# Kernel tuning notes

Hardware: AMD Instinct MI355X
Metric: run time of the kernel (lower is better)

Reference implementation:

```python
import jax, jax.numpy as jnp
import numpy as np

D_MODEL = 512
D_VALUE = 512
N_HEADS = 8
NEG_INF = -1e30


def _layernorm(x, g, b, eps=1e-5):
    mu = jnp.mean(x, axis=-1, keepdims=True)
    var = jnp.var(x, axis=-1, keepdims=True)
    return (x - mu) * jax.lax.rsqrt(var + eps) * g + b


def setup_inputs() -> dict:
    key = jax.random.key(0)
    ks = jax.random.split(key, 16)
    B, L, dq = 4, 2048, 512
    d_model, d_value, H = D_MODEL, D_VALUE, N_HEADS
    d4 = 4 * d_model
    s = lambda d: 1.0 / np.sqrt(d)
    inp = {
        "q": jax.random.normal(ks[0], (B, L, dq), jnp.float32),
        "k": jax.random.normal(ks[1], (B, L, dq), jnp.float32),
        "v": jax.random.normal(ks[2], (B, L, d_value), jnp.float32),
        "Wq": jax.random.normal(ks[3], (d_model, dq), jnp.float32) * s(dq),
        "bq": jnp.zeros((d_model,), jnp.float32),
        "Wk": jax.random.normal(ks[4], (d_model, dq), jnp.float32) * s(dq),
        "bk": jnp.zeros((d_model,), jnp.float32),
        "Wv": jax.random.normal(ks[5], (d_model, d_value), jnp.float32) * s(d_value),
        "bv": jnp.zeros((d_model,), jnp.float32),
        "Wo": jax.random.normal(ks[6], (d_value, d_model), jnp.float32) * s(d_model),
        "bo": jnp.zeros((d_value,), jnp.float32),
        "Wc1": jax.random.normal(ks[7], (d4, d_value), jnp.float32) * s(d_value),
        "bc1": jnp.zeros((d4,), jnp.float32),
        "Wc2": jax.random.normal(ks[8], (d_value, d4), jnp.float32) * s(d4),
        "bc2": jnp.zeros((d_value,), jnp.float32),
        "g1": jnp.ones((d_value,), jnp.float32),
        "b1": jnp.zeros((d_value,), jnp.float32),
        "g2": jnp.ones((d_value,), jnp.float32),
        "b2": jnp.zeros((d_value,), jnp.float32),
        "Wl": jax.random.normal(ks[9], (d_model, d_value), jnp.float32) * s(d_value),
        "bl": jnp.zeros((d_model,), jnp.float32),
    }
    return inp


def reference(q, k, v, Wq, bq, Wk, bk, Wv, bv, Wo, bo, Wc1, bc1, Wc2, bc2,
              g1, b1, g2, b2, Wl, bl):
    B, L, _ = q.shape
    S = k.shape[1]
    H = N_HEADS
    E = D_MODEL // H
    # projections -> [B, L, H, E]
    queries = (q @ Wq.T + bq).reshape(B, L, H, E)
    keys = (k @ Wk.T + bk).reshape(B, S, H, E)
    values = (v @ Wv.T + bv).reshape(B, S, H, E)
    # naive causal attention, full [B,H,L,S] scores
    scale = 1.0 / np.sqrt(E)
    scores = jnp.einsum('blhe,bshe->bhls', queries, keys)
    causal = jnp.triu(jnp.ones((L, S), dtype=bool), k=1)  # True above diagonal
    scores = jnp.where(causal, NEG_INF, scores)
    A = jax.nn.softmax(scale * scores, axis=-1)
    att = jnp.einsum('bhls,bshd->blhd', A, values).reshape(B, L, H * E)
    att = att @ Wo.T + bo
    # residual + FFN (conv1d kernel_size=1 == pointwise linear)
    x = _layernorm(v + att, g1, b1)
    y = jax.nn.relu(x @ Wc1.T + bc1)
    y = y @ Wc2.T + bc2
    y = _layernorm(x + y, g2, b2)
    return y @ Wl.T + bl
```

## Files before the change

kernel.cpp:

```cpp
#include <hip/hip_runtime.h>
#include <hip/hip_bf16.h>


typedef __attribute__((ext_vector_type(8))) short sh8;
typedef __attribute__((ext_vector_type(4))) float f32x4;

#define QSCALE 0.18033688011110543f

__device__ __forceinline__ void storeOut(float* p, float v) { *p = v; }
__device__ __forceinline__ void storeOut(__hip_bfloat16* p, float v) { *p = __float2bfloat16(v); }

__device__ __forceinline__ void gl_lds16(const void* g, void* l) {
    __builtin_amdgcn_global_load_lds((const __attribute__((address_space(1))) void*)g,
                                     (__attribute__((address_space(3))) void*)l, 16, 0, 0);
}

__device__ __forceinline__ unsigned pk_bf16(float a, float b) {
    __hip_bfloat162 h = __float22bfloat162_rn(make_float2(a, b));
    return *(unsigned*)&h;
}
__device__ __forceinline__ sh8 pk8(float4 a, float4 b) {
    int4 iv = make_int4(pk_bf16(a.x, a.y), pk_bf16(a.z, a.w),
                        pk_bf16(b.x, b.y), pk_bf16(b.z, b.w));
    return *(sh8*)&iv;
}

struct WArg { const float* w[7]; unsigned short* wd; };
__global__ __launch_bounds__(256) void conv_w(WArg p)
{
    const int i = (blockIdx.x * 256 + threadIdx.x) * 4;
    if (i >= 3407872) return;
    const float* s; int off;
    if      (i < 262144)  { s = p.w[0]; off = i; }
    else if (i < 524288)  { s = p.w[1]; off = i - 262144; }
    else if (i < 786432)  { s = p.w[2]; off = i - 524288; }
    else if (i < 1048576) { s = p.w[3]; off = i - 786432; }
    else if (i < 1310720) { s = p.w[4]; off = i - 1048576; }
    else if (i < 2359296) { s = p.w[5]; off = i - 1310720; }
    else                  { s = p.w[6]; off = i - 2359296; }
    const float4 v = *(const float4*)(s + off);
    *(uint2*)(p.wd + i) = make_uint2(pk_bf16(v.x, v.y), pk_bf16(v.z, v.w));
}

struct QkvArg {
    const float *A0, *A1, *A2;
    const float *b0, *b1, *b2;
    unsigned short *C0, *C1;
    unsigned short *Vt;
};
__global__ __launch_bounds__(256) void gemm_qkv(QkvArg ar, const unsigned short* __restrict__ Wall,
                                                int M, int N, int K)
{
    const int z = blockIdx.z;
    const float* A = z == 0 ? ar.A0 : (z == 1 ? ar.A1 : ar.A2);
    const unsigned short* W = Wall + (size_t)z * 262144;
    const float* bias = z == 0 ? ar.b0 : (z == 1 ? ar.b1 : ar.b2);

    __shared__ float AsF[8192];
    __shared__ unsigned short BsL[8192];
    const int t    = threadIdx.x;
    const int wave = t >> 6, lane = t & 63;
    const int quad = lane >> 4, col = lane & 15;
    const int wm   = wave >> 1, wn = wave & 1;
    const int m0   = blockIdx.y * 128, n0 = blockIdx.x * 128;

    f32x4 acc[4][4];
    #pragma unroll
    for (int mt = 0; mt < 4; mt++)
        #pragma unroll
        for (int nt = 0; nt < 4; nt++)
            acc[mt][nt] = (f32x4){0.f, 0.f, 0.f, 0.f};

    for (int k0 = 0; k0 < K; k0 += 64) {
        #pragma unroll
        for (int seg = 0; seg < 8; seg++) {
            const int r0  = (seg * 4 + wave) * 4;
            const int row = r0 + (lane >> 4);
            const int ck  = (lane & 15) ^ (row & 15);
            gl_lds16(A + (size_t)(m0 + row) * K + k0 + ck * 4, &AsF[r0 * 64]);
        }
        #pragma unroll
        for (int seg = 0; seg < 4; seg++) {
            const int r0  = (seg * 4 + wave) * 8;
            const int row = r0 + (lane >> 3);
            const int ck  = (lane & 7) ^ (row & 7);
            gl_lds16(W + (size_t)(n0 + row) * K + k0 + ck * 8, &BsL[r0 * 64]);
        }
        __syncthreads();
        #pragma unroll
        for (int kc = 0; kc < 2; kc++) {
            sh8 af[4], bf[4];
            #pragma unroll
            for (int mt = 0; mt < 4; mt++) {
                const int mr  = wm * 64 + mt * 16 + col;
                const int q0  = kc * 8 + quad * 2;
                const int m16 = mr & 15;
                float4 f0 = *(const float4*)&AsF[mr * 64 + ((q0 ^ m16) << 2)];
                float4 f1 = *(const float4*)&AsF[mr * 64 + (((q0 + 1) ^ m16) << 2)];
                af[mt] = pk8(f0, f1);
            }
            #pragma unroll
            for (int nt = 0; nt < 4; nt++) {
                const int nr = wn * 64 + nt * 16 + col;
                bf[nt] = *(const sh8*)&BsL[nr * 64 + (((kc * 4 + quad) ^ (nr & 7)) << 3)];
            }
            #pragma unroll
            for (int mt = 0; mt < 4; mt++)
                #pragma unroll
                for (int nt = 0; nt < 4; nt++)
                    acc[mt][nt] = __builtin_amdgcn_mfma_f32_16x16x32_bf16(af[mt], bf[nt], acc[mt][nt], 0, 0, 0);
        }
        __syncthreads();
    }

    if (z < 2) {
        unsigned short* C = z == 0 ? ar.C0 : ar.C1;
        const float scale = z == 0 ? QSCALE : 1.0f;
        #pragma unroll
        for (int nt = 0; nt < 4; nt++) {
            const int cn = n0 + wn * 64 + nt * 16 + col;
            const float bj = bias[cn];
            #pragma unroll
            for (int mt = 0; mt < 4; mt++) {
                const int rm = m0 + wm * 64 + mt * 16 + quad * 4;
                #pragma unroll
                for (int reg = 0; reg < 4; reg++)
                    C[(size_t)(rm + reg) * N + cn] =
                        (unsigned short)__bfloat16_as_ushort(__float2bfloat16((acc[mt][nt][reg] + bj) * scale));
            }
        }
    } else {
        const int b = m0 >> 11;
        #pragma unroll
        for (int nt = 0; nt < 4; nt++) {
            const int cn = n0 + wn * 64 + nt * 16 + col;
            const int h = cn >> 6, e = cn & 63;
            const float bj = bias[cn];
            #pragma unroll
            for (int mt = 0; mt < 4; mt++) {
                const int s0r = (m0 + wm * 64 + mt * 16 + quad * 4) & 2047;
                float cv[4];
                #pragma unroll
                for (int reg = 0; reg < 4; reg++) cv[reg] = acc[mt][nt][reg] + bj;
                *(uint2*)(ar.Vt + ((size_t)(b * 8 + h) * 64 + e) * 2048 + s0r) =
                    make_uint2(pk_bf16(cv[0], cv[1]), pk_bf16(cv[2], cv[3]));
            }
        }
    }
}

template <typename TOUT, bool RELU>
__global__ __launch_bounds__(256) void gemm_mfma(const unsigned short* __restrict__ A,
                                                 const unsigned short* __restrict__ W,
                                                 const float* __restrict__ bias,
                                                 TOUT* __restrict__ C,
                                                 int M, int N, int K)
{
    __shared__ unsigned short AsL[8192];
    __shared__ unsigned short BsL[8192];
    const int t    = threadIdx.x;
    const int wave = t >> 6, lane = t & 63;
    const int quad = lane >> 4, col = lane & 15;
    const int wm   = wave >> 1, wn = wave & 1;
    const int m0   = blockIdx.y * 128, n0 = blockIdx.x * 128;

    f32x4 acc[4][4];
    #pragma unroll
    for (int mt = 0; mt < 4; mt++)
        #pragma unroll
        for (int nt = 0; nt < 4; nt++)
            acc[mt][nt] = (f32x4){0.f, 0.f, 0.f, 0.f};

    for (int k0 = 0; k0 < K; k0 += 64) {
        #pragma unroll
        for (int seg = 0; seg < 4; seg++) {
            const int r0  = (seg * 4 + wave) * 8;
            const int row = r0 + (lane >> 3);
            const int ck  = (lane & 7) ^ (row & 7);
            gl_lds16(A + (size_t)(m0 + row) * K + k0 + ck * 8, &AsL[r0 * 64]);
            gl_lds16(W + (size_t)(n0 + row) * K + k0 + ck * 8, &BsL[r0 * 64]);
        }
        __syncthreads();
        #pragma unroll
        for (int kc = 0; kc < 2; kc++) {
            sh8 af[4], bf[4];
            #pragma unroll
            for (int mt = 0; mt < 4; mt++) {
                const int ar = wm * 64 + mt * 16 + col;
                af[mt] = *(const sh8*)&AsL[ar * 64 + (((kc * 4 + quad) ^ (ar & 7)) << 3)];
            }
            #pragma unroll
            for (int nt = 0; nt < 4; nt++) {
                const int nr = wn * 64 + nt * 16 + col;
                bf[nt] = *(const sh8*)&BsL[nr * 64 + (((kc * 4 + quad) ^ (nr & 7)) << 3)];
            }
            #pragma unroll
            for (int mt = 0; mt < 4; mt++)
                #pragma unroll
                for (int nt = 0; nt < 4; nt++)
                    acc[mt][nt] = __builtin_amdgcn_mfma_f32_16x16x32_bf16(af[mt], bf[nt], acc[mt][nt], 0, 0, 0);
        }
        __syncthreads();
    }
    #pragma unroll
    for (int nt = 0; nt < 4; nt++) {
        const int cn = n0 + wn * 64 + nt * 16 + col;
        const float bj = bias[cn];
        #pragma unroll
        for (int mt = 0; mt < 4; mt++) {
            const int rm = m0 + wm * 64 + mt * 16 + quad * 4;
            #pragma unroll
            for (int reg = 0; reg < 4; reg++) {
                float cv = acc[mt][nt][reg] + bj;
                if (RELU) cv = fmaxf(cv, 0.f);
                storeOut(&C[(size_t)(rm + reg) * N + cn], cv);
            }
        }
    }
}

template <typename TOUT, bool RELU>
__global__ __launch_bounds__(256) void gemm_mfma64(const unsigned short* __restrict__ A,
                                                   const unsigned short* __restrict__ W,
                                                   const float* __restrict__ bias,
                                                   TOUT* __restrict__ C,
                                                   int M, int N, int K)
{
    __shared__ unsigned short AsL[4096];
    __shared__ unsigned short BsL[8192];
    const int t    = threadIdx.x;
    const int wave = t >> 6, lane = t & 63;
    const int quad = lane >> 4, col = lane & 15;
    const int wm   = wave >> 1, wn = wave & 1;
    const int m0   = blockIdx.y * 64, n0 = blockIdx.x * 128;

    f32x4 acc[2][4];
    #pragma unroll
    for (int mt = 0; mt < 2; mt++)
        #pragma unroll
        for (int nt = 0; nt < 4; nt++)
            acc[mt][nt] = (f32x4){0.f, 0.f, 0.f, 0.f};

    for (int k0 = 0; k0 < K; k0 += 64) {
        #pragma unroll
        for (int seg = 0; seg < 2; seg++) {
            const int r0  = (seg * 4 + wave) * 8;
            const int row = r0 + (lane >> 3);
            const int ck  = (lane & 7) ^ (row & 7);
            gl_lds16(A + (size_t)(m0 + row) * K + k0 + ck * 8, &AsL[r0 * 64]);
        }
        #pragma unroll
        for (int seg = 0; seg < 4; seg++) {
            const int r0  = (seg * 4 + wave) * 8;
            const int row = r0 + (lane >> 3);
            const int ck  = (lane & 7) ^ (row & 7);
            gl_lds16(W + (size_t)(n0 + row) * K + k0 + ck * 8, &BsL[r0 * 64]);
        }
        __syncthreads();
        #pragma unroll
        for (int kc = 0; kc < 2; kc++) {
            sh8 af[2], bf[4];
            #pragma unroll
            for (int mt = 0; mt < 2; mt++) {
                const int ar = wm * 32 + mt * 16 + col;
                af[mt] = *(const sh8*)&AsL[ar * 64 + (((kc * 4 + quad) ^ (ar & 7)) << 3)];
            }
            #pragma unroll
            for (int nt = 0; nt < 4; nt++) {
                const int nr = wn * 64 + nt * 16 + col;
                bf[nt] = *(const sh8*)&BsL[nr * 64 + (((kc * 4 + quad) ^ (nr & 7)) << 3)];
            }
            #pragma unroll
            for (int mt = 0; mt < 2; mt++)
                #pragma unroll
                for (int nt = 0; nt < 4; nt++)
                    acc[mt][nt] = __builtin_amdgcn_mfma_f32_16x16x32_bf16(af[mt], bf[nt], acc[mt][nt], 0, 0, 0);
        }
        __syncthreads();
    }
    #pragma unroll
    for (int nt = 0; nt < 4; nt++) {
        const int cn = n0 + wn * 64 + nt * 16 + col;
        const float bj = bias[cn];
        #pragma unroll
        for (int mt = 0; mt < 2; mt++) {
            const int rm = m0 + wm * 32 + mt * 16 + quad * 4;
            #pragma unroll
            for (int reg = 0; reg < 4; reg++) {
                float cv = acc[mt][nt][reg] + bj;
                if (RELU) cv = fmaxf(cv, 0.f);
                storeOut(&C[(size_t)(rm + reg) * N + cn], cv);
            }
        }
    }
}

__global__ __launch_bounds__(256, 2) void attn_mfma(const unsigned short* __restrict__ Qb,
                                                    const unsigned short* __restrict__ Kb,
                                                    const unsigned short* __restrict__ Vt,
                                                    float* __restrict__ Op,
                                                    float* __restrict__ Lp,
                                                    int L)
{
    __shared__ unsigned short Ks[4096];
    __shared__ unsigned short Vs[4096];
    __shared__ unsigned short Ps[4][16][72];

    const int x    = blockIdx.x;
    const int i    = x >> 1;
    const int sp   = x & 1;
    const int bh   = blockIdx.y;
    const int b    = bh >> 3, h = bh & 7;
    const int t    = threadIdx.x;
    const int w    = t >> 6, lane = t & 63;
    const int quad = lane >> 4, col = lane & 15;

    const int qtA = i, qtB = 31 - i;
    const int qrowA = qtA * 64 + w * 16 + col;
    const int qrowB = qtB * 64 + w * 16 + col;
    const int S  = 32 - i;
    const int h0 = (S + 1) >> 1;
    const int r0 = sp ? h0 : 0;
    const int r1 = sp ? S : h0;

    const int srow = lane >> 3;
    const int scp  = lane & 7;

    sh8 qfA[2], qfB[2];
    {
        const size_t qa = ((size_t)(b * L + qrowA) * 8 + h) * 64;
        qfA[0] = *(const sh8*)(Qb + qa + quad * 8);
        qfA[1] = *(const sh8*)(Qb + qa + 32 + quad * 8);
        const size_t qb2 = ((size_t)(b * L + qrowB) * 8 + h) * 64;
        qfB[0] = *(const sh8*)(Qb + qb2 + quad * 8);
        qfB[1] = *(const sh8*)(Qb + qb2 + 32 + quad * 8);
    }

    f32x4 OA[4], OB[4];
    #pragma unroll
    for (int nt = 0; nt < 4; nt++) { OA[nt] = (f32x4){0.f,0.f,0.f,0.f}; OB[nt] = (f32x4){0.f,0.f,0.f,0.f}; }
    float lA = 0.f, lB = 0.f;

    for (int r = r0; r < r1; r++) {
        const int k0 = r * 64;
        #pragma unroll
        for (int seg = 0; seg < 2; seg++) {
            const int rr  = (seg * 4 + w) * 8;
            const int row = rr + srow;
            const int ck  = scp ^ (row & 7);
            gl_lds16(Kb + ((size_t)(b * L + k0 + row) * 8 + h) * 64 + ck * 8, &Ks[rr * 64]);
            gl_lds16(Vt + (size_t)(bh * 64 + row) * L + k0 + ck * 8, &Vs[rr * 64]);
        }
        __syncthreads();

        const bool actA  = (r <= i);
        const bool maskA = (r == i);
        const bool maskB = (r == S - 1);

        f32x4 stA[4], stB[4];
        const f32x4 zz = {0.f, 0.f, 0.f, 0.f};
        #pragma unroll
        for (int ntk = 0; ntk < 4; ntk++) {
            const int key = ntk * 16 + col;
            const int sw  = key & 7;
            sh8 kf0 = *(const sh8*)&Ks[key * 64 + ((quad ^ sw) << 3)];
            sh8 kf1 = *(const sh8*)&Ks[key * 64 + (((quad + 4) ^ sw) << 3)];
            f32x4 aB = __builtin_amdgcn_mfma_f32_16x16x32_bf16(kf0, qfB[0], zz, 0, 0, 0);
            stB[ntk] = __builtin_amdgcn_mfma_f32_16x16x32_bf16(kf1, qfB[1], aB, 0, 0, 0);
            if (actA) {
                f32x4 aA = __builtin_amdgcn_mfma_f32_16x16x32_bf16(kf0, qfA[0], zz, 0, 0, 0);
                stA[ntk] = __builtin_amdgcn_mfma_f32_16x16x32_bf16(kf1, qfA[1], aA, 0, 0, 0);
            }
        }

        {
            if (maskB) {
                #pragma unroll
                for (int ntk = 0; ntk < 4; ntk++)
                    #pragma unroll
                    for (int reg = 0; reg < 4; reg++)
                        if (k0 + ntk * 16 + quad * 4 + reg > qrowB) stB[ntk][reg] = -1e30f;
            }
            #pragma unroll
            for (int ntk = 0; ntk < 4; ntk++) {
                #pragma unroll
                for (int reg = 0; reg < 4; reg++)
                    stB[ntk][reg] = exp2f(stB[ntk][reg]);
                lB += (stB[ntk][0] + stB[ntk][1]) + (stB[ntk][2] + stB[ntk][3]);
                *(uint2*)&Ps[w][col][ntk * 16 + quad * 4] =
                    make_uint2(pk_bf16(stB[ntk][0], stB[ntk][1]), pk_bf16(stB[ntk][2], stB[ntk][3]));
            }
            #pragma unroll
            for (int kchunk = 0; kchunk < 2; kchunk++) {
                sh8 pf = *(const sh8*)&Ps[w][col][kchunk * 32 + quad * 8];
                #pragma unroll
                for (int nt = 0; nt < 4; nt++) {
                    const int e = nt * 16 + col;
                    sh8 vf = *(const sh8*)&Vs[e * 64 + (((kchunk * 4 + quad) ^ (e & 7)) << 3)];
                    OB[nt] = __builtin_amdgcn_mfma_f32_16x16x32_bf16(pf, vf, OB[nt], 0, 0, 0);
                }
            }
        }

        if (actA) {
            if (maskA) {
                #pragma unroll
                for (int ntk = 0; ntk < 4; ntk++)
                    #pragma unroll
                    for (int reg = 0; reg < 4; reg++)
                        if (k0 + ntk * 16 + quad * 4 + reg > qrowA) stA[ntk][reg] = -1e30f;
            }
            #pragma unroll
            for (int ntk = 0; ntk < 4; ntk++) {
                #pragma unroll
                for (int reg = 0; reg < 4; reg++)
                    stA[ntk][reg] = exp2f(stA[ntk][reg]);
                lA += (stA[ntk][0] + stA[ntk][1]) + (stA[ntk][2] + stA[ntk][3]);
                *(uint2*)&Ps[w][col][ntk * 16 + quad * 4] =
                    make_uint2(pk_bf16(stA[ntk][0], stA[ntk][1]), pk_bf16(stA[ntk][2], stA[ntk][3]));
            }
            #pragma unroll
            for (int kchunk = 0; kchunk < 2; kchunk++) {
                sh8 pf = *(const sh8*)&Ps[w][col][kchunk * 32 + quad * 8];
                #pragma unroll
                for (int nt = 0; nt < 4; nt++) {
                    const int e = nt * 16 + col;
                    sh8 vf = *(const sh8*)&Vs[e * 64 + (((kchunk * 4 + quad) ^ (e & 7)) << 3)];
                    OA[nt] = __builtin_amdgcn_mfma_f32_16x16x32_bf16(pf, vf, OA[nt], 0, 0, 0);
                }
            }
        }
        __syncthreads();
    }

    lA += __shfl_xor(lA, 16); lA += __shfl_xor(lA, 32);
    lB += __shfl_xor(lB, 16); lB += __shfl_xor(lB, 32);
    {
        float* Od = Op + (size_t)sp * 4194304;
        float* Ld = Lp + (size_t)sp * 65536;
        if (quad == 0) {
            Ld[(size_t)(b * L + qtA * 64 + w * 16 + col) * 8 + h] = lA;
            Ld[(size_t)(b * L + qtB * 64 + w * 16 + col) * 8 + h] = lB;
        }
        #pragma unroll
        for (int reg = 0; reg < 4; reg++) {
            const int qrA = qtA * 64 + w * 16 + quad * 4 + reg;
            const int qrB = qtB * 64 + w * 16 + quad * 4 + reg;
            #pragma unroll
            for (int nt = 0; nt < 4; nt++) {
                Od[((size_t)(b * L + qrA) * 8 + h) * 64 + nt * 16 + col] = OA[nt][reg];
                Od[((size_t)(b * L + qrB) * 8 + h) * 64 + nt * 16 + col] = OB[nt][reg];
            }
        }
    }
}

__global__ __launch_bounds__(256) void attn_combine(const float* __restrict__ Op,
                                                    const float* __restrict__ Lp,
                                                    unsigned short* __restrict__ O)
{
    const int row = blockIdx.x;
    const int t   = threadIdx.x;
    const int e   = t * 2;
    const int h   = e >> 6;
    const float l0 = Lp[(size_t)row * 8 + h];
    const float l1 = Lp[65536 + (size_t)row * 8 + h];
    const float inv = 1.f / (l0 + l1);
    const size_t idx = (size_t)row * 512 + e;
    const float2 o0 = *(const float2*)(Op + idx);
    const float2 o1 = *(const float2*)(Op + 4194304 + idx);
    *(unsigned*)&O[idx] = pk_bf16((o0.x + o1.x) * inv, (o0.y + o1.y) * inv);
}

__global__ __launch_bounds__(256) void layernorm_k(const float* __restrict__ f1,
                                                   const float* __restrict__ f2,
                                                   const float* __restrict__ rb,
                                                   const float* __restrict__ g,
                                                   const float* __restrict__ bb,
                                                   float* __restrict__ out32,
                                                   __hip_bfloat16* __restrict__ out16)
{
    const int row = blockIdx.x;
    const int t   = threadIdx.x;
    const size_t base = (size_t)row * 512;
    const int i0 = t * 2;

    float a0 = f1[base + i0], a1 = f1[base + i0 + 1];
    if (f2) { a0 += f2[base + i0]; a1 += f2[base + i0 + 1]; }
    if (rb) { a0 += rb[base + i0]; a1 += rb[base + i0 + 1]; }

    float s = a0 + a1, ss = a0 * a0 + a1 * a1;
    #pragma unroll
    for (int off = 32; off > 0; off >>= 1) {
        s  += __shfl_xor(s, off);
        ss += __shfl_xor(ss, off);
    }
    __shared__ float red[16];
    const int lane = t & 63, wid = t >> 6;
    if (lane == 0) { red[wid] = s; red[8 + wid] = ss; }
    __syncthreads();
    if (t == 0) {
        const float S  = red[0] + red[1] + red[2] + red[3];
        const float SS = red[8] + red[9] + red[10] + red[11];
        const float mu = S * (1.f / 512.f);
        const float var = SS * (1.f / 512.f) - mu * mu;
        red[0] = mu;
        red[1] = rsqrtf(fmaxf(var, 0.f) + 1e-5f);
    }
    __syncthreads();
    const float mu = red[0], rstd = red[1];
    const float y0 = (a0 - mu) * rstd * g[i0]     + bb[i0];
    const float y1 = (a1 - mu) * rstd * g[i0 + 1] + bb[i0 + 1];
    if (out32) { out32[base + i0] = y0; out32[base + i0 + 1] = y1; }
    if (out16) { out16[base + i0] = __float2bfloat16(y0); out16[base + i0 + 1] = __float2bfloat16(y1); }
}

extern "C" void kernel_launch(void* const* d_in, const int* in_sizes, int n_in,
                              void* d_out, int out_size, void* d_ws, size_t ws_size,
                              hipStream_t stream)
{
    const float* q   = (const float*)d_in[0];
    const float* k   = (const float*)d_in[1];
    const float* v   = (const float*)d_in[2];
    const float* Wq  = (const float*)d_in[3];
    const float* bq  = (const float*)d_in[4];
    const float* Wk  = (const float*)d_in[5];
    const float* bk  = (const float*)d_in[6];
    const float* Wv  = (const float*)d_in[7];
    const float* bv  = (const float*)d_in[8];
    const float* Wo  = (const float*)d_in[9];
    const float* bo  = (const float*)d_in[10];
    const float* Wc1 = (const float*)d_in[11];
    const float* bc1 = (const float*)d_in[12];
    const float* Wc2 = (const float*)d_in[13];
    const float* bc2 = (const float*)d_in[14];
    const float* g1  = (const float*)d_in[15];
    const float* b1  = (const float*)d_in[16];
    const float* g2  = (const float*)d_in[17];
    const float* b2  = (const float*)d_in[18];
    const float* Wl  = (const float*)d_in[19];
    const float* bl  = (const float*)d_in[20];
    float* out = (float*)d_out;

    const int B = 4, L = 2048, H = 8;
    const int M = B * L;

    char* base = (char*)d_ws;
    unsigned short* Wall = (unsigned short*)(base + 0);
    unsigned short* Wob  = (unsigned short*)(base + 1572864);
    unsigned short* Wlb  = (unsigned short*)(base + 2097152);
    unsigned short* Wc1b = (unsigned short*)(base + 2621440);
    unsigned short* Wc2b = (unsigned short*)(base + 4718592);
    unsigned short* Qb   = (unsigned short*)(base + 6815744);
    unsigned short* Kb   = (unsigned short*)(base + 15204352);
    unsigned short* Vt   = (unsigned short*)(base + 23592960);
    unsigned short* A1   = (unsigned short*)(base + 31981568);
    float*          Oprt = (float*)(base + 40370176);
    float*          Lprt = (float*)(base + 73924608);
    float*          A2   = (float*)(base + 40370176);
    float*          X1   = (float*)(base + 57147392);
    unsigned short* X1b  = (unsigned short*)(base + 73924608);
    unsigned short* X2b  = (unsigned short*)(base + 73924608);
    unsigned short* H1   = (unsigned short*)(base + 6815744);
    float*          Y2   = (float*)(base + 40370176);

    const dim3 blk(256);

    WArg wa;
    wa.w[0] = Wq; wa.w[1] = Wk; wa.w[2] = Wv; wa.w[3] = Wo; wa.w[4] = Wl;
    wa.w[5] = Wc1; wa.w[6] = Wc2; wa.wd = Wall;
    conv_w<<<dim3(3328), blk, 0, stream>>>(wa);

    QkvArg qa;
    qa.A0 = q;  qa.A1 = k;  qa.A2 = v;
    qa.b0 = bq; qa.b1 = bk; qa.b2 = bv;
    qa.C0 = Qb; qa.C1 = Kb; qa.Vt = Vt;
    gemm_qkv<<<dim3(4, 64, 3), blk, 0, stream>>>(qa, Wall, M, 512, 512);

    attn_mfma<<<dim3(32, B * H), blk, 0, stream>>>(Qb, Kb, Vt, Oprt, Lprt, L);

    attn_combine<<<dim3(M), blk, 0, stream>>>(Oprt, Lprt, A1);

    gemm_mfma64<float, false><<<dim3(4, 128), blk, 0, stream>>>(A1, Wob, bo, A2, M, 512, 512);

    layernorm_k<<<dim3(M), blk, 0, stream>>>(A2, nullptr, v, g1, b1, X1, (__hip_bfloat16*)X1b);

    gemm_mfma<__hip_bfloat16, true><<<dim3(16, 64), blk, 0, stream>>>(X1b, Wc1b, bc1, (__hip_bfloat16*)H1, M, 2048, 512);

    gemm_mfma64<float, false><<<dim3(4, 128), blk, 0, stream>>>(H1, Wc2b, bc2, Y2, M, 512, 2048);

    layernorm_k<<<dim3(M), blk, 0, stream>>>(X1, Y2, nullptr, g2, b2, nullptr, (__hip_bfloat16*)X2b);

    gemm_mfma64<float, false><<<dim3(4, 128), blk, 0, stream>>>(X2b, Wlb, bl, out, M, 512, 512);
}
```

Before: 330.8 us.

## Double-buffer K/V tiles in attention kernel and raise occupancy hint

The attention kernel now keeps two LDS buffers each for K and V. It prefetches tile r+1 with direct global-to-LDS loads while tile r is being processed, and drops the barrier that used to sit right after each load. This is meant to hide global load latency behind the MFMA and exp work. Launch bounds also go from 2 to 3 blocks per CU, which caps registers more tightly and may cause spills. The extra LDS buffer raises shared memory use, and the compiler may still insert conservative waitcnts that limit the overlap.

After: 329.5 us. Within noise of the previous version (-0.4%).

```diff
diff --git a/kernel.cpp b/kernel.cpp
--- a/kernel.cpp
+++ b/kernel.cpp
@@ -295,15 +295,15 @@
     }
 }
 
-__global__ __launch_bounds__(256, 2) void attn_mfma(const unsigned short* __restrict__ Qb,
+__global__ __launch_bounds__(256, 3) void attn_mfma(const unsigned short* __restrict__ Qb,
                                                     const unsigned short* __restrict__ Kb,
                                                     const unsigned short* __restrict__ Vt,
                                                     float* __restrict__ Op,
                                                     float* __restrict__ Lp,
                                                     int L)
 {
-    __shared__ unsigned short Ks[4096];
-    __shared__ unsigned short Vs[4096];
+    __shared__ unsigned short Ks[2][4096];
+    __shared__ unsigned short Vs[2][4096];
     __shared__ unsigned short Ps[4][16][72];
 
     const int x    = blockIdx.x;
@@ -341,18 +341,34 @@
     for (int nt = 0; nt < 4; nt++) { OA[nt] = (f32x4){0.f,0.f,0.f,0.f}; OB[nt] = (f32x4){0.f,0.f,0.f,0.f}; }
     float lA = 0.f, lB = 0.f;
 
-    for (int r = r0; r < r1; r++) {
-        const int k0 = r * 64;
+    {
+        const int k0 = r0 * 64;
         #pragma unroll
         for (int seg = 0; seg < 2; seg++) {
             const int rr  = (seg * 4 + w) * 8;
             const int row = rr + srow;
             const int ck  = scp ^ (row & 7);
-            gl_lds16(Kb + ((size_t)(b * L + k0 + row) * 8 + h) * 64 + ck * 8, &Ks[rr * 64]);
-            gl_lds16(Vt + (size_t)(bh * 64 + row) * L + k0 + ck * 8, &Vs[rr * 64]);
-        }
-        __syncthreads();
-
+            gl_lds16(Kb + ((size_t)(b * L + k0 + row) * 8 + h) * 64 + ck * 8, &Ks[0][rr * 64]);
+            gl_lds16(Vt + (size_t)(bh * 64 + row) * L + k0 + ck * 8, &Vs[0][rr * 64]);
+        }
+        __syncthreads();
+    }
+
+    int cur = 0;
+    for (int r = r0; r < r1; r++) {
+        if (r + 1 < r1) {
+            const int k1 = (r + 1) * 64;
+            #pragma unroll
+            for (int seg = 0; seg < 2; seg++) {
+                const int rr  = (seg * 4 + w) * 8;
+                const int row = rr + srow;
+                const int ck  = scp ^ (row & 7);
+                gl_lds16(Kb + ((size_t)(b * L + k1 + row) * 8 + h) * 64 + ck * 8, &Ks[cur ^ 1][rr * 64]);
+                gl_lds16(Vt + (size_t)(bh * 64 + row) * L + k1 + ck * 8, &Vs[cur ^ 1][rr * 64]);
+            }
+        }
+
+        const int k0 = r * 64;
         const bool actA  = (r <= i);
         const bool maskA = (r == i);
         const bool maskB = (r == S - 1);
@@ -363,8 +379,8 @@
         for (int ntk = 0; ntk < 4; ntk++) {
             const int key = ntk * 16 + col;
             const int sw  = key & 7;
-            sh8 kf0 = *(const sh8*)&Ks[key * 64 + ((quad ^ sw) << 3)];
-            sh8 kf1 = *(const sh8*)&Ks[key * 64 + (((quad + 4) ^ sw) << 3)];
+            sh8 kf0 = *(const sh8*)&Ks[cur][key * 64 + ((quad ^ sw) << 3)];
+            sh8 kf1 = *(const sh8*)&Ks[cur][key * 64 + (((quad + 4) ^ sw) << 3)];
             f32x4 aB = __builtin_amdgcn_mfma_f32_16x16x32_bf16(kf0, qfB[0], zz, 0, 0, 0);
             stB[ntk] = __builtin_amdgcn_mfma_f32_16x16x32_bf16(kf1, qfB[1], aB, 0, 0, 0);
             if (actA) {
@@ -396,7 +412,7 @@
                 #pragma unroll
                 for (int nt = 0; nt < 4; nt++) {
                     const int e = nt * 16 + col;
-                    sh8 vf = *(const sh8*)&Vs[e * 64 + (((kchunk * 4 + quad) ^ (e & 7)) << 3)];
+                    sh8 vf = *(const sh8*)&Vs[cur][e * 64 + (((kchunk * 4 + quad) ^ (e & 7)) << 3)];
                     OB[nt] = __builtin_amdgcn_mfma_f32_16x16x32_bf16(pf, vf, OB[nt], 0, 0, 0);
                 }
             }
@@ -425,12 +441,13 @@
                 #pragma unroll
                 for (int nt = 0; nt < 4; nt++) {
                     const int e = nt * 16 + col;
-                    sh8 vf = *(const sh8*)&Vs[e * 64 + (((kchunk * 4 + quad) ^ (e & 7)) << 3)];
+                    sh8 vf = *(const sh8*)&Vs[cur][e * 64 + (((kchunk * 4 + quad) ^ (e & 7)) << 3)];
                     OA[nt] = __builtin_amdgcn_mfma_f32_16x16x32_bf16(pf, vf, OA[nt], 0, 0, 0);
                 }
             }
         }
         __syncthreads();
+        cur ^= 1;
     }
 
     lA += __shfl_xor(lA, 16); lA += __shfl_xor(lA, 32);
```
